# Optimization experiments

Hardware: AMD Instinct MI355X
Metric: run time of the kernel (lower is better)

## Reference

```python
import jax, jax.numpy as jnp
import numpy as np

B, S, D, H = 4, 4096, 256, 4
Dh = D // H


def setup_inputs() -> dict:
    key = jax.random.key(0)
    ks = jax.random.split(key, 5)
    scale = 1.0 / np.sqrt(D)
    return {
        "inputs": jax.random.normal(ks[0], (B, S, D), dtype=jnp.float32),
        "Wq": jax.random.normal(ks[1], (D, D), dtype=jnp.float32) * scale,
        "bq": jnp.zeros((D,), jnp.float32),
        "Wk": jax.random.normal(ks[2], (D, D), dtype=jnp.float32) * scale,
        "bk": jnp.zeros((D,), jnp.float32),
        "Wv": jax.random.normal(ks[3], (D, D), dtype=jnp.float32) * scale,
        "bv": jnp.zeros((D,), jnp.float32),
        "Wo": jax.random.normal(ks[4], (D, D), dtype=jnp.float32) * scale,
        "bo": jnp.zeros((D,), jnp.float32),
    }


def reference(inputs, Wq, bq, Wk, bk, Wv, bv, Wo, bo):
    b, s, d = inputs.shape
    # QKV projections
    q = inputs @ Wq + bq
    k = inputs @ Wk + bk
    v = inputs @ Wv + bv
    # separate heads: [B, S, D] -> [B, H, S, Dh]
    def split_heads(x):
        return x.reshape(b, s, H, Dh).transpose(0, 2, 1, 3)
    q, k, v = split_heads(q), split_heads(k), split_heads(v)
    # scaled dot-product attention (no causal mask: mask=False)
    scores = jnp.einsum("bhqd,bhkd->bhqk", q, k) / jnp.sqrt(jnp.float32(Dh))
    weights = jax.nn.softmax(scores, axis=-1)
    attn = jnp.einsum("bhqk,bhkd->bhqd", weights, v)
    # combine heads: [B, H, S, Dh] -> [B, S, D]
    attn = attn.transpose(0, 2, 1, 3).reshape(b, s, d)
    return attn @ Wo + bo
```

## Files before the change

kernel.cpp:

```cpp
#include <hip/hip_runtime.h>
#include <cmath>

#define B_  4
#define S_  4096
#define D_  256
#define H_  4
#define DH_ 64
#define M_TOTAL (B_*S_)
#define QSCALE 0.1803368801111f

typedef __bf16 bf16x8 __attribute__((ext_vector_type(8)));
typedef __bf16 bf16x4 __attribute__((ext_vector_type(4)));
typedef __bf16 bf16x2 __attribute__((ext_vector_type(2)));
typedef float  f32x4  __attribute__((ext_vector_type(4)));
typedef float  f32x16 __attribute__((ext_vector_type(16)));

#define AS1 __attribute__((address_space(1)))
#define AS3 __attribute__((address_space(3)))

__device__ __forceinline__ void g2lds16(const void* g, void* l) {
    __builtin_amdgcn_global_load_lds((AS1 const void*)g, (AS3 void*)l, 16, 0, 0);
}

#if __has_builtin(__builtin_amdgcn_permlane32_swap)
typedef unsigned uint2v __attribute__((ext_vector_type(2)));
__device__ __forceinline__ void plswap(unsigned &a, unsigned &b) {
    uint2v r = __builtin_amdgcn_permlane32_swap(a, b, false, false);
    a = r[0]; b = r[1];
}
#else
__device__ __forceinline__ void plswap(unsigned &a, unsigned &b) {
    unsigned bl = (unsigned)__shfl_xor((int)b, 32);
    unsigned ah = (unsigned)__shfl_xor((int)a, 32);
    bool hi = (threadIdx.x & 32) != 0;
    unsigned na = hi ? bl : a;
    unsigned nb = hi ? b  : ah;
    a = na; b = nb;
}
#endif

__device__ __forceinline__ unsigned pk2(float x, float y) {
    bf16x2 t; t[0] = (__bf16)x; t[1] = (__bf16)y;
    return __builtin_bit_cast(unsigned, t);
}

__global__ __launch_bounds__(256) void prep(const float* __restrict__ X,
                                            const float* __restrict__ W0,
                                            const float* __restrict__ W1,
                                            const float* __restrict__ W2,
                                            const float* __restrict__ W3,
                                            __bf16* __restrict__ Xb,
                                            __bf16* __restrict__ Wt_all) {
    int t = threadIdx.x;
    if (blockIdx.x < 2048) {
        size_t i = ((size_t)blockIdx.x * 256 + t) * 8;
        float4 v0 = *(const float4*)(X + i);
        float4 v1 = *(const float4*)(X + i + 4);
        bf16x8 o;
        o[0] = (__bf16)v0.x; o[1] = (__bf16)v0.y; o[2] = (__bf16)v0.z; o[3] = (__bf16)v0.w;
        o[4] = (__bf16)v1.x; o[5] = (__bf16)v1.y; o[6] = (__bf16)v1.z; o[7] = (__bf16)v1.w;
        *(bf16x8*)(Xb + i) = o;
        return;
    }
    int bid = blockIdx.x - 2048;
    int z = bid >> 6, rem = bid & 63;
    int by = rem >> 3, bx = rem & 7;
    const float* W = (z == 0) ? W0 : (z == 1) ? W1 : (z == 2) ? W2 : W3;
    float wsc = (z == 0) ? QSCALE : 1.0f;
    __bf16* Wt = Wt_all + (size_t)z * 65536;
    __shared__ float tile[32][33];
    int r0 = by * 32, c0 = bx * 32;
#pragma unroll
    for (int e = 0; e < 4; e++) {
        int idx = t + e * 256; int r = idx >> 5, c = idx & 31;
        tile[r][c] = W[(r0 + r) * 256 + c0 + c];
    }
    __syncthreads();
#pragma unroll
    for (int e = 0; e < 4; e++) {
        int idx = t + e * 256; int r = idx >> 5, c = idx & 31;
        Wt[(c0 + r) * 256 + (r0 + c)] = (__bf16)(tile[c][r] * wsc);
    }
}

__global__ __launch_bounds__(256) void gemm_bt(const __bf16* __restrict__ A,
                                               const __bf16* __restrict__ Wt_all,
                                               const float* __restrict__ bias0,
                                               const float* __restrict__ bias1,
                                               const float* __restrict__ bias2,
                                               __bf16* __restrict__ outb,
                                               __bf16* __restrict__ voutb,
                                               float* __restrict__ outf,
                                               int out_is_f32, float bsc0) {
    constexpr int K = 256;
    __shared__ __attribute__((aligned(16))) __bf16 As[128 * 32];
    __shared__ __attribute__((aligned(16))) __bf16 Bs[128 * 32];

    int t = threadIdx.x;
    int lane = t & 63, w = t >> 6;
    int wr = w >> 1, wc = w & 1;
    int l16 = lane & 15, quad = lane >> 4;
    int mbase = blockIdx.x * 128;
    int nbase = blockIdx.y * 128;
    int z = blockIdx.z;
    const __bf16* Bt = Wt_all + (size_t)z * 65536;
    const float* bias = (z == 0) ? bias0 : (z == 1) ? bias1 : bias2;
    float bscale = (z == 0) ? bsc0 : 1.0f;

    f32x4 acc[4][4] = {};

    int srow = t >> 2;
    int sseg = (t & 3) * 8;

    for (int kk = 0; kk < K; kk += 32) {
        __syncthreads();
        g2lds16(A  + (size_t)(mbase +      srow) * K + kk + sseg, (char*)As +        t * 16);
        g2lds16(A  + (size_t)(mbase + 64 + srow) * K + kk + sseg, (char*)As + 4096 + t * 16);
        g2lds16(Bt + (size_t)(nbase +      srow) * K + kk + sseg, (char*)Bs +        t * 16);
        g2lds16(Bt + (size_t)(nbase + 64 + srow) * K + kk + sseg, (char*)Bs + 4096 + t * 16);
        __syncthreads();

        bf16x8 a[4], b[4];
#pragma unroll
        for (int i = 0; i < 4; i++)
            a[i] = *(const bf16x8*)(As + (wr * 64 + i * 16 + l16) * 32 + quad * 8);
#pragma unroll
        for (int j = 0; j < 4; j++)
            b[j] = *(const bf16x8*)(Bs + (wc * 64 + j * 16 + l16) * 32 + quad * 8);
#pragma unroll
        for (int i = 0; i < 4; i++)
#pragma unroll
            for (int j = 0; j < 4; j++)
                acc[i][j] = __builtin_amdgcn_mfma_f32_16x16x32_bf16(a[i], b[j], acc[i][j], 0, 0, 0);
    }

#pragma unroll
    for (int i = 0; i < 4; i++) {
#pragma unroll
        for (int j = 0; j < 4; j++) {
            int col = nbase + wc * 64 + j * 16 + l16;
            float bv = bias[col] * bscale;
            int row0 = mbase + wr * 64 + i * 16 + quad * 4;
            if (out_is_f32) {
#pragma unroll
                for (int r = 0; r < 4; r++)
                    outf[(size_t)(row0 + r) * 256 + col] = acc[i][j][r] + bv;
            } else if (z == 2) {
                int hcol = col >> 6, dh = col & 63;
                int bidx = row0 >> 12, s0 = row0 & 4095;
                bf16x4 pk;
#pragma unroll
                for (int r = 0; r < 4; r++) pk[r] = (__bf16)(acc[i][j][r] + bv);
                *(bf16x4*)(voutb + ((size_t)(bidx * 4 + hcol) * 64 + dh) * 4096 + s0) = pk;
            } else {
#pragma unroll
                for (int r = 0; r < 4; r++)
                    outb[(size_t)z * ((size_t)M_TOTAL * 256) + (size_t)(row0 + r) * 256 + col] =
                        (__bf16)(acc[i][j][r] + bv);
            }
        }
    }
}

__global__ __launch_bounds__(128) void attn(const __bf16* __restrict__ Qb,
                                            const __bf16* __restrict__ Kb,
                                            const __bf16* __restrict__ Vt,
                                            __bf16* __restrict__ Ctx) {
    __shared__ __attribute__((aligned(16))) __bf16 smem[9216];
    __bf16* Ks = smem;
    __bf16* Vs = smem + 4096;

    int t = threadIdx.x;
    int lane = t & 63, w = t >> 6;
    int l31 = lane & 31, hh = lane >> 5;

    int lin = blockIdx.x;
    int xcd = lin & 7, j = lin >> 3;
    int bh = xcd * 2 + (j & 1);
    int qblk = j >> 1;
    int b = bh >> 2, hd = bh & 3;
    int qw = qblk * 128 + w * 64;

    bf16x8 qf[4][2];
#pragma unroll
    for (int ks = 0; ks < 4; ks++)
#pragma unroll
        for (int qt = 0; qt < 2; qt++)
            qf[ks][qt] = *(const bf16x8*)(Qb + (size_t)(b * S_ + qw + qt * 32 + l31) * 256
                                              + hd * 64 + ks * 16 + hh * 8);

    f32x16 acc[2][2] = {};
    float lsum[2] = {0.f, 0.f};

    int srow = t >> 3;
    int sseg = t & 7;

    for (int kv = 0; kv < S_; kv += 64) {
        __syncthreads();
#pragma unroll
        for (int c = 0; c < 4; c++) {
            int rr = c * 16 + srow;
            int gseg = (sseg ^ (rr & 7)) * 8;
            g2lds16(Kb + (size_t)(b * S_ + kv + rr) * 256 + hd * 64 + gseg,
                    (char*)smem + c * 2048 + t * 16);
            g2lds16(Vt + ((size_t)bh * 64 + rr) * S_ + kv + gseg,
                    (char*)smem + 8192 + c * 2048 + t * 16);
        }
        __syncthreads();

        f32x16 st[2][2] = {};
#pragma unroll
        for (int kt = 0; kt < 2; kt++) {
            bf16x8 kf[4];
#pragma unroll
            for (int ks = 0; ks < 4; ks++) {
                int slot = (ks * 2 + hh) ^ (l31 & 7);
                kf[ks] = *(const bf16x8*)(Ks + (kt * 32 + l31) * 64 + slot * 8);
            }
#pragma unroll
            for (int ks = 0; ks < 4; ks++)
#pragma unroll
                for (int qt = 0; qt < 2; qt++)
                    st[kt][qt] = __builtin_amdgcn_mfma_f32_32x32x16_bf16(kf[ks], qf[ks][qt], st[kt][qt], 0, 0, 0);
        }

#pragma unroll
        for (int kt = 0; kt < 2; kt++) {
            unsigned dd[2][8];
#pragma unroll
            for (int qt = 0; qt < 2; qt++) {
                float p[16];
#pragma unroll
                for (int r = 0; r < 16; r++) p[r] = __builtin_amdgcn_exp2f(st[kt][qt][r]);
                float s0 = ((p[0] + p[1]) + (p[2] + p[3])) + ((p[4] + p[5]) + (p[6] + p[7]));
                float s1 = ((p[8] + p[9]) + (p[10] + p[11])) + ((p[12] + p[13]) + (p[14] + p[15]));
                lsum[qt] += s0 + s1;
#pragma unroll
                for (int m = 0; m < 4; m++) {
                    dd[qt][m * 2]     = pk2(p[4 * m],     p[4 * m + 1]);
                    dd[qt][m * 2 + 1] = pk2(p[4 * m + 2], p[4 * m + 3]);
                }
            }
#pragma unroll
            for (int tt = 0; tt < 2; tt++) {
                int tks = kt * 2 + tt;
                bf16x8 pf[2];
#pragma unroll
                for (int qt = 0; qt < 2; qt++) {
                    unsigned x0 = dd[qt][4 * tt],     y0 = dd[qt][4 * tt + 2];
                    unsigned x1 = dd[qt][4 * tt + 1], y1 = dd[qt][4 * tt + 3];
                    plswap(x0, y0);
                    plswap(x1, y1);
                    union { unsigned u[4]; bf16x8 v; } c;
                    c.u[0] = x0; c.u[1] = x1; c.u[2] = y0; c.u[3] = y1;
                    pf[qt] = c.v;
                }
#pragma unroll
                for (int mt = 0; mt < 2; mt++) {
                    int slot = (tks * 2 + hh) ^ (l31 & 7);
                    bf16x8 vf = *(const bf16x8*)(Vs + (mt * 32 + l31) * 64 + slot * 8);
#pragma unroll
                    for (int qt = 0; qt < 2; qt++)
                        acc[mt][qt] = __builtin_amdgcn_mfma_f32_32x32x16_bf16(vf, pf[qt], acc[mt][qt], 0, 0, 0);
                }
            }
        }
    }

    float inv[2];
#pragma unroll
    for (int qt = 0; qt < 2; qt++) {
        float l = lsum[qt];
        l += __shfl_xor(l, 32);
        inv[qt] = 1.f / l;
    }

    __syncthreads();
    __bf16* Es = smem + w * 4608;
#pragma unroll
    for (int qt = 0; qt < 2; qt++)
#pragma unroll
        for (int mt = 0; mt < 2; mt++)
#pragma unroll
            for (int rg = 0; rg < 4; rg++) {
                bf16x4 ov;
#pragma unroll
                for (int e = 0; e < 4; e++) ov[e] = (__bf16)(acc[mt][qt][4 * rg + e] * inv[qt]);
                int dhb = mt * 32 + rg * 8 + 4 * hh;
                *(bf16x4*)(Es + (qt * 32 + l31) * 72 + dhb) = ov;
            }
    __syncthreads();
#pragma unroll
    for (int pass = 0; pass < 8; pass++) {
        int q = pass * 8 + (lane >> 3);
        int col = (lane & 7) * 8;
        bf16x8 val = *(const bf16x8*)(Es + q * 72 + col);
        *(bf16x8*)(Ctx + (size_t)(b * S_ + qw + q) * 256 + hd * 64 + col) = val;
    }
}

extern "C" void kernel_launch(void* const* d_in, const int* in_sizes, int n_in,
                              void* d_out, int out_size, void* d_ws, size_t ws_size,
                              hipStream_t stream) {
    const float* X  = (const float*)d_in[0];
    const float* Wq = (const float*)d_in[1];
    const float* bq = (const float*)d_in[2];
    const float* Wk = (const float*)d_in[3];
    const float* bk = (const float*)d_in[4];
    const float* Wv = (const float*)d_in[5];
    const float* bv = (const float*)d_in[6];
    const float* Wo = (const float*)d_in[7];
    const float* bo = (const float*)d_in[8];
    float* out = (float*)d_out;

    char* ws = (char*)d_ws;
    const size_t MB = 1024 * 1024;
    __bf16* Xb  = (__bf16*)(ws);
    __bf16* Ctx = (__bf16*)(ws);
    __bf16* Wt  = (__bf16*)(ws + 8 * MB);
    __bf16* Qb  = (__bf16*)(ws + 8 * MB + 512 * 1024);
    __bf16* Kb  = (__bf16*)((char*)Qb + 8 * MB);
    __bf16* Vt  = (__bf16*)((char*)Kb + 8 * MB);

    prep<<<dim3(2304), dim3(256), 0, stream>>>(X, Wq, Wk, Wv, Wo, Xb, Wt);
    gemm_bt<<<dim3(M_TOTAL / 128, 2, 3), dim3(256), 0, stream>>>(
        Xb, Wt, bq, bk, bv, Qb, Vt, nullptr, 0, QSCALE);
    attn<<<dim3(512), dim3(128), 0, stream>>>(Qb, Kb, Vt, Ctx);
    gemm_bt<<<dim3(M_TOTAL / 128, 2, 1), dim3(256), 0, stream>>>(
        Ctx, Wt + 3 * 65536, bo, bo, bo, nullptr, nullptr, out, 1, 1.0f);
}
```

Measured before the change: 199.4 us.

## Split KV range across the two waves of each attention block

Each attention block now serves 64 queries instead of 128. Its two waves share the same queries, and each wave walks alternate 64-key tiles into its own private LDS buffer. That removes the block-wide __syncthreads inside the KV loop in favour of per-wave waitcnt, and the grid doubles to 1024 blocks. At the end, wave 1 dumps its partial accumulators and row sums to LDS, and wave 0 merges them, normalises and writes the context. The trade-off is twice the total K/V loading per query, an extra cross-wave reduction, and wave 1 sitting idle during the epilogue.

```diff
diff --git a/kernel.cpp b/kernel.cpp
--- a/kernel.cpp
+++ b/kernel.cpp
@@ -166,9 +166,7 @@
                                             const __bf16* __restrict__ Kb,
                                             const __bf16* __restrict__ Vt,
                                             __bf16* __restrict__ Ctx) {
-    __shared__ __attribute__((aligned(16))) __bf16 smem[9216];
-    __bf16* Ks = smem;
-    __bf16* Vs = smem + 4096;
+    __shared__ __attribute__((aligned(16))) __bf16 smem[16384];
 
     int t = threadIdx.x;
     int lane = t & 63, w = t >> 6;
@@ -179,7 +177,13 @@
     int bh = xcd * 2 + (j & 1);
     int qblk = j >> 1;
     int b = bh >> 2, hd = bh & 3;
-    int qw = qblk * 128 + w * 64;
+    int qw = qblk * 64;
+
+    char* myK = (char*)smem + w * 16384 / 2 * 2;
+    myK = (char*)smem + (size_t)w * 16384;
+    char* myV = myK + 8192;
+    __bf16* Ksp = (__bf16*)myK;
+    __bf16* Vsp = (__bf16*)myV;
 
     bf16x8 qf[4][2];
 #pragma unroll
@@ -192,21 +196,21 @@
     f32x16 acc[2][2] = {};
     float lsum[2] = {0.f, 0.f};
 
-    int srow = t >> 3;
-    int sseg = t & 7;
-
-    for (int kv = 0; kv < S_; kv += 64) {
-        __syncthreads();
-#pragma unroll
-        for (int c = 0; c < 4; c++) {
-            int rr = c * 16 + srow;
+    int srow = lane >> 3;
+    int sseg = lane & 7;
+
+    for (int kv = 64 * w; kv < S_; kv += 128) {
+        asm volatile("s_waitcnt lgkmcnt(0)" ::: "memory");
+#pragma unroll
+        for (int c = 0; c < 8; c++) {
+            int rr = c * 8 + srow;
             int gseg = (sseg ^ (rr & 7)) * 8;
             g2lds16(Kb + (size_t)(b * S_ + kv + rr) * 256 + hd * 64 + gseg,
-                    (char*)smem + c * 2048 + t * 16);
+                    myK + c * 1024 + lane * 16);
             g2lds16(Vt + ((size_t)bh * 64 + rr) * S_ + kv + gseg,
-                    (char*)smem + 8192 + c * 2048 + t * 16);
-        }
-        __syncthreads();
+                    myV + c * 1024 + lane * 16);
+        }
+        asm volatile("s_waitcnt vmcnt(0)" ::: "memory");
 
         f32x16 st[2][2] = {};
 #pragma unroll
@@ -215,7 +219,7 @@
 #pragma unroll
             for (int ks = 0; ks < 4; ks++) {
                 int slot = (ks * 2 + hh) ^ (l31 & 7);
-                kf[ks] = *(const bf16x8*)(Ks + (kt * 32 + l31) * 64 + slot * 8);
+                kf[ks] = *(const bf16x8*)(Ksp + (kt * 32 + l31) * 64 + slot * 8);
             }
 #pragma unroll
             for (int ks = 0; ks < 4; ks++)
@@ -258,7 +262,7 @@
 #pragma unroll
                 for (int mt = 0; mt < 2; mt++) {
                     int slot = (tks * 2 + hh) ^ (l31 & 7);
-                    bf16x8 vf = *(const bf16x8*)(Vs + (mt * 32 + l31) * 64 + slot * 8);
+                    bf16x8 vf = *(const bf16x8*)(Vsp + (mt * 32 + l31) * 64 + slot * 8);
 #pragma unroll
                     for (int qt = 0; qt < 2; qt++)
                         acc[mt][qt] = __builtin_amdgcn_mfma_f32_32x32x16_bf16(vf, pf[qt], acc[mt][qt], 0, 0, 0);
@@ -267,35 +271,68 @@
         }
     }
 
-    float inv[2];
-#pragma unroll
-    for (int qt = 0; qt < 2; qt++) {
-        float l = lsum[qt];
-        l += __shfl_xor(l, 32);
-        inv[qt] = 1.f / l;
-    }
+#pragma unroll
+    for (int qt = 0; qt < 2; qt++)
+        lsum[qt] += __shfl_xor(lsum[qt], 32);
 
     __syncthreads();
-    __bf16* Es = smem + w * 4608;
-#pragma unroll
-    for (int qt = 0; qt < 2; qt++)
+    float* lsdump = (float*)((char*)smem + 16384);
+    if (w == 1) {
 #pragma unroll
         for (int mt = 0; mt < 2; mt++)
 #pragma unroll
-            for (int rg = 0; rg < 4; rg++) {
-                bf16x4 ov;
-#pragma unroll
-                for (int e = 0; e < 4; e++) ov[e] = (__bf16)(acc[mt][qt][4 * rg + e] * inv[qt]);
-                int dhb = mt * 32 + rg * 8 + 4 * hh;
-                *(bf16x4*)(Es + (qt * 32 + l31) * 72 + dhb) = ov;
-            }
+            for (int qt = 0; qt < 2; qt++)
+#pragma unroll
+                for (int g = 0; g < 4; g++) {
+                    int idx = (mt * 2 + qt) * 4 + g;
+                    f32x4 v;
+#pragma unroll
+                    for (int e = 0; e < 4; e++) v[e] = acc[mt][qt][4 * g + e];
+                    *(f32x4*)((char*)smem + idx * 1024 + lane * 16) = v;
+                }
+        lsdump[lane * 2]     = lsum[0];
+        lsdump[lane * 2 + 1] = lsum[1];
+    }
     __syncthreads();
-#pragma unroll
-    for (int pass = 0; pass < 8; pass++) {
-        int q = pass * 8 + (lane >> 3);
-        int col = (lane & 7) * 8;
-        bf16x8 val = *(const bf16x8*)(Es + q * 72 + col);
-        *(bf16x8*)(Ctx + (size_t)(b * S_ + qw + q) * 256 + hd * 64 + col) = val;
+    if (w == 0) {
+        float inv[2];
+#pragma unroll
+        for (int qt = 0; qt < 2; qt++)
+            inv[qt] = 1.f / (lsum[qt] + lsdump[lane * 2 + qt]);
+#pragma unroll
+        for (int mt = 0; mt < 2; mt++)
+#pragma unroll
+            for (int qt = 0; qt < 2; qt++)
+#pragma unroll
+                for (int g = 0; g < 4; g++) {
+                    int idx = (mt * 2 + qt) * 4 + g;
+                    f32x4 v = *(const f32x4*)((char*)smem + idx * 1024 + lane * 16);
+#pragma unroll
+                    for (int e = 0; e < 4; e++) acc[mt][qt][4 * g + e] += v[e];
+                }
+
+        __bf16* Es = (__bf16*)((char*)smem + 16896);
+#pragma unroll
+        for (int qt = 0; qt < 2; qt++)
+#pragma unroll
+            for (int mt = 0; mt < 2; mt++)
+#pragma unroll
+                for (int rg = 0; rg < 4; rg++) {
+                    bf16x4 ov;
+#pragma unroll
+                    for (int e = 0; e < 4; e++)
+                        ov[e] = (__bf16)(acc[mt][qt][4 * rg + e] * inv[qt]);
+                    int dhb = mt * 32 + rg * 8 + 4 * hh;
+                    *(bf16x4*)(Es + (qt * 32 + l31) * 72 + dhb) = ov;
+                }
+        asm volatile("s_waitcnt lgkmcnt(0)" ::: "memory");
+#pragma unroll
+        for (int pass = 0; pass < 8; pass++) {
+            int q = pass * 8 + (lane >> 3);
+            int col = (lane & 7) * 8;
+            bf16x8 val = *(const bf16x8*)(Es + q * 72 + col);
+            *(bf16x8*)(Ctx + (size_t)(b * S_ + qw + q) * 256 + hd * 64 + col) = val;
+        }
     }
 }
 
@@ -325,7 +362,7 @@
     prep<<<dim3(2304), dim3(256), 0, stream>>>(X, Wq, Wk, Wv, Wo, Xb, Wt);
     gemm_bt<<<dim3(M_TOTAL / 128, 2, 3), dim3(256), 0, stream>>>(
         Xb, Wt, bq, bk, bv, Qb, Vt, nullptr, 0, QSCALE);
-    attn<<<dim3(512), dim3(128), 0, stream>>>(Qb, Kb, Vt, Ctx);
+    attn<<<dim3(1024), dim3(128), 0, stream>>>(Qb, Kb, Vt, Ctx);
     gemm_bt<<<dim3(M_TOTAL / 128, 2, 1), dim3(256), 0, stream>>>(
         Ctx, Wt + 3 * 65536, bo, bo, bo, nullptr, nullptr, out, 1, 1.0f);
 }
```

Measured after the change: 198.1 us. Within noise of the previous version (-0.7%).

## Make attention single-wave per block with double-buffered async K/V staging

Applied to the files above, without the earlier changes.

Each attention block now holds one 64-lane wavefront covering 64 queries, launched as twice as many blocks. K/V tiles are double-buffered in LDS: the next tile is issued with global_load_lds before the current one is consumed, and the wait uses explicit vmcnt counts instead of block barriers. The aim is to hide global load latency behind the MFMA and softmax work and to drop __syncthreads. The cost is that each wave now fetches its own K/V tiles instead of sharing them with a sibling wave, which doubles L2 traffic for K/V and raises LDS use per block.

```diff
diff --git a/kernel.cpp b/kernel.cpp
--- a/kernel.cpp
+++ b/kernel.cpp
@@ -162,16 +162,13 @@
     }
 }
 
-__global__ __launch_bounds__(128) void attn(const __bf16* __restrict__ Qb,
-                                            const __bf16* __restrict__ Kb,
-                                            const __bf16* __restrict__ Vt,
-                                            __bf16* __restrict__ Ctx) {
-    __shared__ __attribute__((aligned(16))) __bf16 smem[9216];
-    __bf16* Ks = smem;
-    __bf16* Vs = smem + 4096;
-
-    int t = threadIdx.x;
-    int lane = t & 63, w = t >> 6;
+__global__ __launch_bounds__(64) void attn(const __bf16* __restrict__ Qb,
+                                           const __bf16* __restrict__ Kb,
+                                           const __bf16* __restrict__ Vt,
+                                           __bf16* __restrict__ Ctx) {
+    __shared__ __attribute__((aligned(16))) __bf16 smem[16384];
+
+    int lane = threadIdx.x & 63;
     int l31 = lane & 31, hh = lane >> 5;
 
     int lin = blockIdx.x;
@@ -179,7 +176,10 @@
     int bh = xcd * 2 + (j & 1);
     int qblk = j >> 1;
     int b = bh >> 2, hd = bh & 3;
-    int qw = qblk * 128 + w * 64;
+    int qw = qblk * 64;
+
+    const __bf16* Kbase = Kb + (size_t)b * S_ * 256 + hd * 64;
+    const __bf16* Vbase = Vt + (size_t)bh * 64 * S_;
 
     bf16x8 qf[4][2];
 #pragma unroll
@@ -192,21 +192,35 @@
     f32x16 acc[2][2] = {};
     float lsum[2] = {0.f, 0.f};
 
-    int srow = t >> 3;
-    int sseg = t & 7;
-
-    for (int kv = 0; kv < S_; kv += 64) {
-        __syncthreads();
-#pragma unroll
-        for (int c = 0; c < 4; c++) {
-            int rr = c * 16 + srow;
-            int gseg = (sseg ^ (rr & 7)) * 8;
-            g2lds16(Kb + (size_t)(b * S_ + kv + rr) * 256 + hd * 64 + gseg,
-                    (char*)smem + c * 2048 + t * 16);
-            g2lds16(Vt + ((size_t)bh * 64 + rr) * S_ + kv + gseg,
-                    (char*)smem + 8192 + c * 2048 + t * 16);
+    int srow = lane >> 3;
+    int sseg = lane & 7;
+
+#define STAGE(kv, buf) do {                                                    \
+        char* mk = (char*)smem + (buf) * 16384;                                \
+        char* mv = mk + 8192;                                                  \
+        _Pragma("unroll")                                                      \
+        for (int c = 0; c < 8; c++) {                                          \
+            int rr = c * 8 + srow;                                             \
+            int gseg = (sseg ^ (rr & 7)) * 8;                                  \
+            g2lds16(Kbase + (size_t)((kv) + rr) * 256 + gseg,                  \
+                    mk + c * 1024 + lane * 16);                                \
+            g2lds16(Vbase + (size_t)rr * S_ + (kv) + gseg,                     \
+                    mv + c * 1024 + lane * 16);                                \
+        }                                                                      \
+    } while (0)
+
+    STAGE(0, 0);
+
+    for (int it = 0; it < 64; it++) {
+        int buf = it & 1;
+        if (it < 63) {
+            STAGE((it + 1) * 64, buf ^ 1);
+            asm volatile("s_waitcnt vmcnt(16)" ::: "memory");
+        } else {
+            asm volatile("s_waitcnt vmcnt(0)" ::: "memory");
         }
-        __syncthreads();
+        __bf16* Ksp = (__bf16*)((char*)smem + buf * 16384);
+        __bf16* Vsp = (__bf16*)((char*)smem + buf * 16384 + 8192);
 
         f32x16 st[2][2] = {};
 #pragma unroll
@@ -215,7 +229,7 @@
 #pragma unroll
             for (int ks = 0; ks < 4; ks++) {
                 int slot = (ks * 2 + hh) ^ (l31 & 7);
-                kf[ks] = *(const bf16x8*)(Ks + (kt * 32 + l31) * 64 + slot * 8);
+                kf[ks] = *(const bf16x8*)(Ksp + (kt * 32 + l31) * 64 + slot * 8);
             }
 #pragma unroll
             for (int ks = 0; ks < 4; ks++)
@@ -258,7 +272,7 @@
 #pragma unroll
                 for (int mt = 0; mt < 2; mt++) {
                     int slot = (tks * 2 + hh) ^ (l31 & 7);
-                    bf16x8 vf = *(const bf16x8*)(Vs + (mt * 32 + l31) * 64 + slot * 8);
+                    bf16x8 vf = *(const bf16x8*)(Vsp + (mt * 32 + l31) * 64 + slot * 8);
 #pragma unroll
                     for (int qt = 0; qt < 2; qt++)
                         acc[mt][qt] = __builtin_amdgcn_mfma_f32_32x32x16_bf16(vf, pf[qt], acc[mt][qt], 0, 0, 0);
@@ -266,6 +280,7 @@
             }
         }
     }
+#undef STAGE
 
     float inv[2];
 #pragma unroll
@@ -275,8 +290,7 @@
         inv[qt] = 1.f / l;
     }
 
-    __syncthreads();
-    __bf16* Es = smem + w * 4608;
+    __bf16* Es = smem;
 #pragma unroll
     for (int qt = 0; qt < 2; qt++)
 #pragma unroll
@@ -285,11 +299,11 @@
             for (int rg = 0; rg < 4; rg++) {
                 bf16x4 ov;
 #pragma unroll
-                for (int e = 0; e < 4; e++) ov[e] = (__bf16)(acc[mt][qt][4 * rg + e] * inv[qt]);
+                for (int e = 0; e < 4; e++)
+                    ov[e] = (__bf16)(acc[mt][qt][4 * rg + e] * inv[qt]);
                 int dhb = mt * 32 + rg * 8 + 4 * hh;
                 *(bf16x4*)(Es + (qt * 32 + l31) * 72 + dhb) = ov;
             }
-    __syncthreads();
 #pragma unroll
     for (int pass = 0; pass < 8; pass++) {
         int q = pass * 8 + (lane >> 3);
@@ -325,7 +339,7 @@
     prep<<<dim3(2304), dim3(256), 0, stream>>>(X, Wq, Wk, Wv, Wo, Xb, Wt);
     gemm_bt<<<dim3(M_TOTAL / 128, 2, 3), dim3(256), 0, stream>>>(
         Xb, Wt, bq, bk, bv, Qb, Vt, nullptr, 0, QSCALE);
-    attn<<<dim3(512), dim3(128), 0, stream>>>(Qb, Kb, Vt, Ctx);
+    attn<<<dim3(1024), dim3(64), 0, stream>>>(Qb, Kb, Vt, Ctx);
     gemm_bt<<<dim3(M_TOTAL / 128, 2, 1), dim3(256), 0, stream>>>(
         Ctx, Wt + 3 * 65536, bo, bo, bo, nullptr, nullptr, out, 1, 1.0f);
 }
```

New measurement: 201.2 us. About the same (+0.9%).
